# Kernel tuning notes

Measured on AMD Instinct MI355X. Metric: run time of the kernel, lower is better.

The kernel has to match this reference:

```python
import jax, jax.numpy as jnp
import numpy as np

B, S, H, A, V = 128, 128, 1024, 1024, 50000
NEG = -1e11  # mask value used by the original for zero scores (padded positions)


def setup_inputs() -> dict:
    key = jax.random.key(0)
    ks = jax.random.split(key, 10)
    b_ih = jnp.zeros((4 * H,), jnp.float32).at[H:2 * H].set(1.0)  # forget_bias
    b_hh = jnp.zeros((4 * H,), jnp.float32).at[H:2 * H].set(1.0)
    return {
        "input": jax.random.randint(ks[0], (B,), 0, V),
        "prev_h": jax.random.normal(ks[1], (B, H), jnp.float32),
        "prev_c": jax.random.normal(ks[2], (B, H), jnp.float32),
        "encoder_output": jax.random.normal(ks[3], (B, S, H), jnp.float32),
        "emb": jax.random.normal(ks[4], (V, H), jnp.float32) * 0.02,
        "W_ih": jax.random.normal(ks[5], (4 * H, H), jnp.float32) * 0.02,
        "W_hh": jax.random.normal(ks[6], (4 * H, H), jnp.float32) * 0.02,
        "b_ih": b_ih,
        "b_hh": b_hh,
        "W_out": jax.random.normal(ks[7], (A, 2 * H), jnp.float32) * 0.02,
        "b_out": jnp.zeros((A,), jnp.float32),
        "W_out2": jax.random.normal(ks[8], (V, A), jnp.float32) * 0.02,
        "b_out2": jnp.zeros((V,), jnp.float32),
    }


def reference(input, prev_h, prev_c, encoder_output, emb, W_ih, W_hh, b_ih, b_hh,
              W_out, b_out, W_out2, b_out2):
    # embedding lookup (dropout p=0 -> identity)
    x = emb[input]  # [B, H]
    # LSTMCell, PyTorch gate order (i, f, g, o)
    gates = x @ W_ih.T + b_ih + prev_h @ W_hh.T + b_hh  # [B, 4H]
    i, f, g, o = jnp.split(gates, 4, axis=-1)
    c = jax.nn.sigmoid(f) * prev_c + jax.nn.sigmoid(i) * jnp.tanh(g)
    h = jax.nn.sigmoid(o) * jnp.tanh(c)
    # dot attention over (padded) encoder outputs
    scores = jnp.einsum("bsh,bh->bs", encoder_output, h)  # [B, S]
    scores = jnp.where(scores == 0, NEG, scores)          # mask padded rows
    attn = jax.nn.softmax(scores, axis=1)
    context = jnp.einsum("bsh,bs->bh", encoder_output, attn)  # [B, H]
    # MLP decode
    attention_vector = jnp.tanh(jnp.concatenate([context, h], axis=-1) @ W_out.T + b_out)
    logits = attention_vector @ W_out2.T + b_out2  # [B, V]
    output = jax.nn.log_softmax(logits, axis=1)
    return output, h, c
```

## Files before the change

### kernel.cpp

```cpp
#include <hip/hip_runtime.h>
#include <hip/hip_bf16.h>
#include <math.h>

#define Bn 128
#define Sn 128
#define Hn 1024
#define Vn 50000

using short8  = __attribute__((ext_vector_type(8))) short;
using floatx4 = __attribute__((ext_vector_type(4))) float;

__device__ __forceinline__ unsigned short f2bf_bits(float f) {
  union { __hip_bfloat16 h; unsigned short u; } cv;
  cv.h = __float2bfloat16(f);
  return cv.u;
}
__device__ __forceinline__ float bf_bits2f(unsigned short u) {
  union { __hip_bfloat16 h; unsigned short u; } cv;
  cv.u = u;
  return __bfloat162float(cv.h);
}
__device__ __forceinline__ short8 cvt8(float4 a, float4 b) {
  short8 r;
  r[0]=(short)f2bf_bits(a.x); r[1]=(short)f2bf_bits(a.y);
  r[2]=(short)f2bf_bits(a.z); r[3]=(short)f2bf_bits(a.w);
  r[4]=(short)f2bf_bits(b.x); r[5]=(short)f2bf_bits(b.y);
  r[6]=(short)f2bf_bits(b.z); r[7]=(short)f2bf_bits(b.w);
  return r;
}
__device__ __forceinline__ void split8(float4 a, float4 b, short8& hi, short8& lo) {
  float f[8] = {a.x,a.y,a.z,a.w,b.x,b.y,b.z,b.w};
#pragma unroll
  for (int i=0;i<8;++i) {
    unsigned short h = f2bf_bits(f[i]);
    hi[i] = (short)h;
    lo[i] = (short)f2bf_bits(f[i] - bf_bits2f(h));
  }
}
__device__ __forceinline__ floatx4 mfma16(short8 a, short8 b, floatx4 c) {
  return __builtin_amdgcn_mfma_f32_16x16x32_bf16(a, b, c, 0, 0, 0);
}

__global__ void __launch_bounds__(256) k1_pack(const int* __restrict__ inp,
    const float* __restrict__ prev_h, const float* __restrict__ emb,
    unsigned short* __restrict__ xh_hi, unsigned short* __restrict__ xh_lo) {
  int idx = blockIdx.x*256 + threadIdx.x;
  int b = idx >> 11, k = idx & 2047;
  if (k < 1024) {
    float v = emb[(size_t)inp[b]*Hn + k];
    xh_hi[idx] = f2bf_bits(v);
  } else {
    float v = prev_h[b*Hn + (k-1024)];
    unsigned short hi = f2bf_bits(v);
    xh_hi[idx] = hi;
    xh_lo[b*Hn + (k-1024)] = f2bf_bits(v - bf_bits2f(hi));
  }
}

__global__ void __launch_bounds__(64) k2_gates(
    const unsigned short* __restrict__ xh_hi, const unsigned short* __restrict__ xh_lo,
    const float* __restrict__ W_ih, const float* __restrict__ W_hh,
    const float* __restrict__ b_ih, const float* __restrict__ b_hh,
    float* __restrict__ gates) {
  int lane = threadIdx.x, l15 = lane & 15, quad = lane >> 4;
  int n = blockIdx.x*16 + l15;
  floatx4 z = {0.f,0.f,0.f,0.f};
  floatx4 acc[8];
#pragma unroll
  for (int t=0;t<8;++t) acc[t] = z;

  for (int k0 = 0; k0 < 1024; k0 += 32) {
    int k = k0 + quad*8;
    const float* wp = W_ih + (size_t)n*Hn + k;
    float4 w0 = *(const float4*)wp;
    float4 w1 = *(const float4*)(wp+4);
    short8 bfrag = cvt8(w0,w1);
#pragma unroll
    for (int t=0;t<8;++t) {
      short8 afrag = *(const short8*)(xh_hi + (t*16 + l15)*2048 + k);
      acc[t] = mfma16(afrag, bfrag, acc[t]);
    }
  }
  for (int k0 = 0; k0 < 1024; k0 += 32) {
    int k = k0 + quad*8;
    const float* wp = W_hh + (size_t)n*Hn + k;
    float4 w0 = *(const float4*)wp;
    float4 w1 = *(const float4*)(wp+4);
    short8 whi, wlo; split8(w0,w1,whi,wlo);
#pragma unroll
    for (int t=0;t<8;++t) {
      short8 ahi = *(const short8*)(xh_hi + (t*16 + l15)*2048 + 1024 + k);
      short8 alo = *(const short8*)(xh_lo + (t*16 + l15)*1024 + k);
      acc[t] = mfma16(ahi, whi, acc[t]);
      acc[t] = mfma16(alo, whi, acc[t]);
      acc[t] = mfma16(ahi, wlo, acc[t]);
    }
  }
  float bias = b_ih[n] + b_hh[n];
#pragma unroll
  for (int t=0;t<8;++t)
#pragma unroll
    for (int r=0;r<4;++r) {
      int m = t*16 + quad*4 + r;
      gates[m*4096 + n] = acc[t][r] + bias;
    }
}

__global__ void __launch_bounds__(256) k3_lstm(const float* __restrict__ gates,
    const float* __restrict__ prev_c, float* __restrict__ out,
    float* __restrict__ h32, unsigned short* __restrict__ ctxh) {
  int idx = blockIdx.x*256 + threadIdx.x;
  int b = idx >> 10, k = idx & 1023;
  const float* g = gates + b*4096;
  float gi = g[k], gf = g[k+1024], gg = g[k+2048], go = g[k+3072];
  float si = 1.f/(1.f+expf(-gi));
  float sf = 1.f/(1.f+expf(-gf));
  float so = 1.f/(1.f+expf(-go));
  float c = sf*prev_c[idx] + si*tanhf(gg);
  float h = so*tanhf(c);
  out[6400000 + idx] = h;
  out[6531072 + idx] = c;
  h32[idx] = h;
  ctxh[b*2048 + 1024 + k] = f2bf_bits(h);
}

__global__ void __launch_bounds__(256) k4a_scores(const float* __restrict__ enc,
    const float* __restrict__ h32, float* __restrict__ scores) {
  int w = blockIdx.x*4 + (threadIdx.x>>6);
  int lane = threadIdx.x & 63;
  int b = w >> 7, s = w & 127;
  const float* e = enc + (size_t)(b*Sn + s)*Hn;
  const float* hp = h32 + b*Hn;
  float sum = 0.f;
#pragma unroll
  for (int j=0;j<4;++j) {
    int k = j*256 + lane*4;
    float4 ev = *(const float4*)(e+k);
    float4 hv = *(const float4*)(hp+k);
    sum += ev.x*hv.x + ev.y*hv.y + ev.z*hv.z + ev.w*hv.w;
  }
#pragma unroll
  for (int o=32;o>0;o>>=1) sum += __shfl_xor(sum, o, 64);
  if (lane==0) {
    if (sum == 0.f) sum = -1e11f;
    scores[b*Sn+s] = sum;
  }
}

__global__ void __launch_bounds__(256) k4b_ctx(const float* __restrict__ enc,
    const float* __restrict__ scores, unsigned short* __restrict__ ctxh) {
  __shared__ float sc[128];
  __shared__ float red[128];
  int tid = threadIdx.x, b = blockIdx.y;
  if (tid < 128) { float v = scores[b*Sn+tid]; sc[tid] = v; red[tid] = v; }
  __syncthreads();
  for (int st=64; st>0; st>>=1) {
    if (tid<st) red[tid] = fmaxf(red[tid], red[tid+st]);
    __syncthreads();
  }
  float mx = red[0];
  __syncthreads();
  if (tid<128) { float e = expf(sc[tid]-mx); sc[tid]=e; red[tid]=e; }
  __syncthreads();
  for (int st=64; st>0; st>>=1) {
    if (tid<st) red[tid] += red[tid+st];
    __syncthreads();
  }
  float inv = 1.0f/red[0];
  __syncthreads();
  if (tid<128) sc[tid] *= inv;
  __syncthreads();
  int hcol = blockIdx.x*256 + tid;
  const float* e = enc + (size_t)b*(Sn*Hn) + hcol;
  float acc = 0.f;
#pragma unroll 8
  for (int s2=0; s2<128; ++s2) acc += sc[s2]*e[(size_t)s2*Hn];
  ctxh[b*2048 + hcol] = f2bf_bits(acc);
}

__global__ void __launch_bounds__(64) k5_att(const unsigned short* __restrict__ ctxh,
    const float* __restrict__ W_out, const float* __restrict__ b_out,
    unsigned short* __restrict__ av) {
  int lane = threadIdx.x, l15 = lane&15, quad = lane>>6 ? 0 : lane>>4;
  quad = lane >> 4;
  int n = blockIdx.x*16 + l15;
  int mbase = blockIdx.y*64;
  floatx4 z = {0.f,0.f,0.f,0.f};
  floatx4 acc[4];
#pragma unroll
  for (int t=0;t<4;++t) acc[t]=z;
  for (int k0=0;k0<2048;k0+=32) {
    int k = k0 + quad*8;
    const float* wp = W_out + (size_t)n*2048 + k;
    float4 w0=*(const float4*)wp, w1=*(const float4*)(wp+4);
    short8 bfrag = cvt8(w0,w1);
#pragma unroll
    for (int t=0;t<4;++t) {
      short8 afrag = *(const short8*)(ctxh + (mbase + t*16 + l15)*2048 + k);
      acc[t] = mfma16(afrag, bfrag, acc[t]);
    }
  }
  float bias = b_out[n];
#pragma unroll
  for (int t=0;t<4;++t)
#pragma unroll
    for (int r=0;r<4;++r) {
      int m = mbase + t*16 + quad*4 + r;
      av[m*Hn + n] = f2bf_bits(tanhf(acc[t][r] + bias));
    }
}

__global__ void __launch_bounds__(64) k6a_logits(const unsigned short* __restrict__ av,
    const float* __restrict__ W2, const float* __restrict__ b2,
    float* __restrict__ out) {
  int lane = threadIdx.x, l15 = lane&15, quad = lane>>4;
  int v = blockIdx.x*16 + l15;
  floatx4 z = {0.f,0.f,0.f,0.f};
  floatx4 acc[8];
#pragma unroll
  for (int t=0;t<8;++t) acc[t]=z;
  for (int k0=0;k0<1024;k0+=32) {
    int k = k0 + quad*8;
    const float* wp = W2 + (size_t)v*Hn + k;
    float4 w0=*(const float4*)wp, w1=*(const float4*)(wp+4);
    short8 bfrag = cvt8(w0,w1);
#pragma unroll
    for (int t=0;t<8;++t) {
      short8 afrag = *(const short8*)(av + (t*16 + l15)*Hn + k);
      acc[t] = mfma16(afrag, bfrag, acc[t]);
    }
  }
  float bias = b2[v];
#pragma unroll
  for (int t=0;t<8;++t)
#pragma unroll
    for (int r=0;r<4;++r) {
      int m = t*16 + quad*4 + r;
      out[(size_t)m*Vn + v] = acc[t][r] + bias;
    }
}

__global__ void __launch_bounds__(256) k6b_lse(const float* __restrict__ logits,
    float* __restrict__ lse) {
  int b = blockIdx.x, tid = threadIdx.x;
  const float* row = logits + (size_t)b*Vn;
  float m = -3.4e38f, s = 0.f;
  for (int v = tid; v < Vn; v += 256) {
    float x = row[v];
    float nm = fmaxf(m, x);
    s = s*expf(m-nm) + expf(x-nm);
    m = nm;
  }
  __shared__ float sm[256], ss[256];
  sm[tid]=m; ss[tid]=s;
  __syncthreads();
  for (int st=128; st>0; st>>=1) {
    if (tid<st) {
      float m1=sm[tid], m2=sm[tid+st];
      float nm=fmaxf(m1,m2);
      ss[tid]=ss[tid]*expf(m1-nm)+ss[tid+st]*expf(m2-nm);
      sm[tid]=nm;
    }
    __syncthreads();
  }
  if (tid==0) lse[b] = sm[0] + logf(ss[0]);
}

__global__ void __launch_bounds__(256) k6c_sub(float* __restrict__ out,
    const float* __restrict__ lse) {
  int f = blockIdx.x*256 + threadIdx.x;
  if (f >= 12500) return;
  int b = blockIdx.y;
  float l = lse[b];
  float4* p = (float4*)(out + (size_t)b*Vn) + f;
  float4 v = *p;
  v.x -= l; v.y -= l; v.z -= l; v.w -= l;
  *p = v;
}

extern "C" void kernel_launch(void* const* d_in, const int* in_sizes, int n_in,
                              void* d_out, int out_size, void* d_ws, size_t ws_size,
                              hipStream_t stream) {
  const int*   inp    = (const int*)d_in[0];
  const float* prev_h = (const float*)d_in[1];
  const float* prev_c = (const float*)d_in[2];
  const float* enc    = (const float*)d_in[3];
  const float* emb    = (const float*)d_in[4];
  const float* W_ih   = (const float*)d_in[5];
  const float* W_hh   = (const float*)d_in[6];
  const float* b_ih   = (const float*)d_in[7];
  const float* b_hh   = (const float*)d_in[8];
  const float* W_out  = (const float*)d_in[9];
  const float* b_out  = (const float*)d_in[10];
  const float* W_out2 = (const float*)d_in[11];
  const float* b_out2 = (const float*)d_in[12];
  float* out = (float*)d_out;
  char* ws = (char*)d_ws;

  unsigned short* xh_hi = (unsigned short*)(ws + 0);
  unsigned short* xh_lo = (unsigned short*)(ws + 524288);
  float* gates          = (float*)(ws + 786432);
  float* h32            = (float*)(ws + 2883584);
  float* scores         = (float*)(ws + 3407872);
  unsigned short* ctxh  = (unsigned short*)(ws + 3473408);
  unsigned short* av    = (unsigned short*)(ws + 3997696);
  float* lse            = (float*)(ws + 4259840);

  k1_pack   <<<1024, 256, 0, stream>>>(inp, prev_h, emb, xh_hi, xh_lo);
  k2_gates  <<<256, 64, 0, stream>>>(xh_hi, xh_lo, W_ih, W_hh, b_ih, b_hh, gates);
  k3_lstm   <<<512, 256, 0, stream>>>(gates, prev_c, out, h32, ctxh);
  k4a_scores<<<4096, 256, 0, stream>>>(enc, h32, scores);
  k4b_ctx   <<<dim3(4,128), 256, 0, stream>>>(enc, scores, ctxh);
  k5_att    <<<dim3(64,2), 64, 0, stream>>>(ctxh, W_out, b_out, av);
  k6a_logits<<<3125, 64, 0, stream>>>(av, W_out2, b_out2, out);
  k6b_lse   <<<128, 256, 0, stream>>>(out, lse);
  k6c_sub   <<<dim3(49,128), 256, 0, stream>>>(out, lse);
}
```

Baseline: 751.0 us.

## Split GEMM batch tiles across blocks, LDS-tile logits GEMM, two-stage LSE

The gates and attention GEMMs now split the batch dimension across grid blocks, so there are more small blocks in flight, each working on one 16-row tile. The logits GEMM becomes a 256-thread block that stages activation and weight tiles through double-buffered LDS, so one block covers 64 vocabulary columns against all 128 batch rows. The log-sum-exp becomes a two-pass reduction spread over 8 chunks per row, which adds parallelism to a pass that previously ran one block per row. In exchange, the gates and attention kernels reload each weight fragment once per batch tile, which multiplies weight traffic, and the logits loop adds LDS barriers.

```diff
diff --git a/kernel.cpp b/kernel.cpp
--- a/kernel.cpp
+++ b/kernel.cpp
@@ -64,10 +64,8 @@
     float* __restrict__ gates) {
   int lane = threadIdx.x, l15 = lane & 15, quad = lane >> 4;
   int n = blockIdx.x*16 + l15;
-  floatx4 z = {0.f,0.f,0.f,0.f};
-  floatx4 acc[8];
-#pragma unroll
-  for (int t=0;t<8;++t) acc[t] = z;
+  int mt = blockIdx.y;
+  floatx4 acc = {0.f,0.f,0.f,0.f};
 
   for (int k0 = 0; k0 < 1024; k0 += 32) {
     int k = k0 + quad*8;
@@ -75,11 +73,8 @@
     float4 w0 = *(const float4*)wp;
     float4 w1 = *(const float4*)(wp+4);
     short8 bfrag = cvt8(w0,w1);
-#pragma unroll
-    for (int t=0;t<8;++t) {
-      short8 afrag = *(const short8*)(xh_hi + (t*16 + l15)*2048 + k);
-      acc[t] = mfma16(afrag, bfrag, acc[t]);
-    }
+    short8 afrag = *(const short8*)(xh_hi + (mt*16 + l15)*2048 + k);
+    acc = mfma16(afrag, bfrag, acc);
   }
   for (int k0 = 0; k0 < 1024; k0 += 32) {
     int k = k0 + quad*8;
@@ -87,23 +82,18 @@
     float4 w0 = *(const float4*)wp;
     float4 w1 = *(const float4*)(wp+4);
     short8 whi, wlo; split8(w0,w1,whi,wlo);
-#pragma unroll
-    for (int t=0;t<8;++t) {
-      short8 ahi = *(const short8*)(xh_hi + (t*16 + l15)*2048 + 1024 + k);
-      short8 alo = *(const short8*)(xh_lo + (t*16 + l15)*1024 + k);
-      acc[t] = mfma16(ahi, whi, acc[t]);
-      acc[t] = mfma16(alo, whi, acc[t]);
-      acc[t] = mfma16(ahi, wlo, acc[t]);
-    }
+    short8 ahi = *(const short8*)(xh_hi + (mt*16 + l15)*2048 + 1024 + k);
+    short8 alo = *(const short8*)(xh_lo + (mt*16 + l15)*1024 + k);
+    acc = mfma16(ahi, whi, acc);
+    acc = mfma16(alo, whi, acc);
+    acc = mfma16(ahi, wlo, acc);
   }
   float bias = b_ih[n] + b_hh[n];
 #pragma unroll
-  for (int t=0;t<8;++t)
-#pragma unroll
-    for (int r=0;r<4;++r) {
-      int m = t*16 + quad*4 + r;
-      gates[m*4096 + n] = acc[t][r] + bias;
-    }
+  for (int r=0;r<4;++r) {
+    int m = mt*16 + quad*4 + r;
+    gates[m*4096 + n] = acc[r] + bias;
+  }
 }
 
 __global__ void __launch_bounds__(256) k3_lstm(const float* __restrict__ gates,
@@ -181,71 +171,105 @@
 __global__ void __launch_bounds__(64) k5_att(const unsigned short* __restrict__ ctxh,
     const float* __restrict__ W_out, const float* __restrict__ b_out,
     unsigned short* __restrict__ av) {
-  int lane = threadIdx.x, l15 = lane&15, quad = lane>>6 ? 0 : lane>>4;
-  quad = lane >> 4;
+  int lane = threadIdx.x, l15 = lane&15, quad = lane>>4;
   int n = blockIdx.x*16 + l15;
-  int mbase = blockIdx.y*64;
-  floatx4 z = {0.f,0.f,0.f,0.f};
-  floatx4 acc[4];
-#pragma unroll
-  for (int t=0;t<4;++t) acc[t]=z;
+  int mt = blockIdx.y;
+  floatx4 acc = {0.f,0.f,0.f,0.f};
   for (int k0=0;k0<2048;k0+=32) {
     int k = k0 + quad*8;
     const float* wp = W_out + (size_t)n*2048 + k;
     float4 w0=*(const float4*)wp, w1=*(const float4*)(wp+4);
     short8 bfrag = cvt8(w0,w1);
-#pragma unroll
-    for (int t=0;t<4;++t) {
-      short8 afrag = *(const short8*)(ctxh + (mbase + t*16 + l15)*2048 + k);
-      acc[t] = mfma16(afrag, bfrag, acc[t]);
-    }
+    short8 afrag = *(const short8*)(ctxh + (mt*16 + l15)*2048 + k);
+    acc = mfma16(afrag, bfrag, acc);
   }
   float bias = b_out[n];
 #pragma unroll
-  for (int t=0;t<4;++t)
-#pragma unroll
-    for (int r=0;r<4;++r) {
-      int m = mbase + t*16 + quad*4 + r;
-      av[m*Hn + n] = f2bf_bits(tanhf(acc[t][r] + bias));
-    }
-}
-
-__global__ void __launch_bounds__(64) k6a_logits(const unsigned short* __restrict__ av,
+  for (int r=0;r<4;++r) {
+    int m = mt*16 + quad*4 + r;
+    av[m*Hn + n] = f2bf_bits(tanhf(acc[r] + bias));
+  }
+}
+
+__global__ void __launch_bounds__(256) k6a_logits(const unsigned short* __restrict__ av,
     const float* __restrict__ W2, const float* __restrict__ b2,
     float* __restrict__ out) {
-  int lane = threadIdx.x, l15 = lane&15, quad = lane>>4;
-  int v = blockIdx.x*16 + l15;
+  __shared__ unsigned short lA[2][128*40];
+  __shared__ unsigned short lB[2][64*40];
+  int tid = threadIdx.x;
+  int wave = tid>>6, lane = tid&63, l15 = lane&15, quad = lane>>4;
+  int tileN = blockIdx.x*64;
+
+  int arow = tid>>2, apart = tid&3;
+  int brow = tid>>3, bpart = tid&7;
+
+  uint4 aR0, aR1; float4 wR0, wR1;
+
+  auto gload = [&](int k0) {
+    aR0 = *(const uint4*)(av + (size_t)arow*Hn + k0 + apart*8);
+    aR1 = *(const uint4*)(av + (size_t)(arow+64)*Hn + k0 + apart*8);
+    int r0 = tileN + brow;      if (r0 > Vn-1) r0 = Vn-1;
+    int r1 = tileN + brow + 32; if (r1 > Vn-1) r1 = Vn-1;
+    wR0 = *(const float4*)(W2 + (size_t)r0*Hn + k0 + bpart*4);
+    wR1 = *(const float4*)(W2 + (size_t)r1*Hn + k0 + bpart*4);
+  };
+  auto lstore = [&](int buf) {
+    *(uint4*)(&lA[buf][arow*40 + apart*8])      = aR0;
+    *(uint4*)(&lA[buf][(arow+64)*40 + apart*8]) = aR1;
+    ushort4 p0, p1;
+    p0.x=f2bf_bits(wR0.x); p0.y=f2bf_bits(wR0.y); p0.z=f2bf_bits(wR0.z); p0.w=f2bf_bits(wR0.w);
+    p1.x=f2bf_bits(wR1.x); p1.y=f2bf_bits(wR1.y); p1.z=f2bf_bits(wR1.z); p1.w=f2bf_bits(wR1.w);
+    *(ushort4*)(&lB[buf][brow*40 + bpart*4])      = p0;
+    *(ushort4*)(&lB[buf][(brow+32)*40 + bpart*4]) = p1;
+  };
+
   floatx4 z = {0.f,0.f,0.f,0.f};
   floatx4 acc[8];
 #pragma unroll
   for (int t=0;t<8;++t) acc[t]=z;
-  for (int k0=0;k0<1024;k0+=32) {
-    int k = k0 + quad*8;
-    const float* wp = W2 + (size_t)v*Hn + k;
-    float4 w0=*(const float4*)wp, w1=*(const float4*)(wp+4);
-    short8 bfrag = cvt8(w0,w1);
-#pragma unroll
-    for (int t=0;t<8;++t) {
-      short8 afrag = *(const short8*)(av + (t*16 + l15)*Hn + k);
-      acc[t] = mfma16(afrag, bfrag, acc[t]);
+
+  gload(0);
+  lstore(0);
+  __syncthreads();
+
+  for (int kc=0; kc<32; ++kc) {
+    int cur = kc&1;
+    if (kc<31) gload((kc+1)*32);
+    short8 bfrag = *(const short8*)(&lB[cur][(wave*16+l15)*40 + quad*8]);
+    short8 af[8];
+#pragma unroll
+    for (int t=0;t<8;++t)
+      af[t] = *(const short8*)(&lA[cur][(t*16+l15)*40 + quad*8]);
+#pragma unroll
+    for (int t=0;t<8;++t)
+      acc[t] = mfma16(af[t], bfrag, acc[t]);
+    if (kc<31) {
+      __syncthreads();
+      lstore(1-cur);
+      __syncthreads();
     }
   }
-  float bias = b2[v];
-#pragma unroll
-  for (int t=0;t<8;++t)
-#pragma unroll
-    for (int r=0;r<4;++r) {
-      int m = t*16 + quad*4 + r;
-      out[(size_t)m*Vn + v] = acc[t][r] + bias;
-    }
-}
-
-__global__ void __launch_bounds__(256) k6b_lse(const float* __restrict__ logits,
-    float* __restrict__ lse) {
-  int b = blockIdx.x, tid = threadIdx.x;
+
+  int n = tileN + wave*16 + l15;
+  if (n < Vn) {
+    float bias = b2[n];
+#pragma unroll
+    for (int t=0;t<8;++t)
+#pragma unroll
+      for (int r=0;r<4;++r) {
+        int m = t*16 + quad*4 + r;
+        out[(size_t)m*Vn + n] = acc[t][r] + bias;
+      }
+  }
+}
+
+__global__ void __launch_bounds__(256) k6b1_lse(const float* __restrict__ logits,
+    float* __restrict__ pm, float* __restrict__ ps) {
+  int b = blockIdx.y, c = blockIdx.x, tid = threadIdx.x;
+  int v0 = c*6250, v1 = v0 + 6250;
   const float* row = logits + (size_t)b*Vn;
   float m = -3.4e38f, s = 0.f;
-  for (int v = tid; v < Vn; v += 256) {
+  for (int v = v0 + tid; v < v1; v += 256) {
     float x = row[v];
     float nm = fmaxf(m, x);
     s = s*expf(m-nm) + expf(x-nm);
@@ -263,7 +287,21 @@
     }
     __syncthreads();
   }
-  if (tid==0) lse[b] = sm[0] + logf(ss[0]);
+  if (tid==0) { pm[b*8+c]=sm[0]; ps[b*8+c]=ss[0]; }
+}
+
+__global__ void __launch_bounds__(128) k6b2_lse(const float* __restrict__ pm,
+    const float* __restrict__ ps, float* __restrict__ lse) {
+  int b = threadIdx.x;
+  float m = -3.4e38f, s = 0.f;
+#pragma unroll
+  for (int c=0;c<8;++c) {
+    float m2 = pm[b*8+c], s2 = ps[b*8+c];
+    float nm = fmaxf(m, m2);
+    s = s*expf(m-nm) + s2*expf(m2-nm);
+    m = nm;
+  }
+  lse[b] = m + logf(s);
 }
 
 __global__ void __launch_bounds__(256) k6c_sub(float* __restrict__ out,
@@ -305,14 +343,17 @@
   unsigned short* ctxh  = (unsigned short*)(ws + 3473408);
   unsigned short* av    = (unsigned short*)(ws + 3997696);
   float* lse            = (float*)(ws + 4259840);
+  float* pm             = (float*)(ws + 4260352);
+  float* ps             = (float*)(ws + 4264448);
 
   k1_pack   <<<1024, 256, 0, stream>>>(inp, prev_h, emb, xh_hi, xh_lo);
-  k2_gates  <<<256, 64, 0, stream>>>(xh_hi, xh_lo, W_ih, W_hh, b_ih, b_hh, gates);
+  k2_gates  <<<dim3(256,8), 64, 0, stream>>>(xh_hi, xh_lo, W_ih, W_hh, b_ih, b_hh, gates);
   k3_lstm   <<<512, 256, 0, stream>>>(gates, prev_c, out, h32, ctxh);
   k4a_scores<<<4096, 256, 0, stream>>>(enc, h32, scores);
   k4b_ctx   <<<dim3(4,128), 256, 0, stream>>>(enc, scores, ctxh);
-  k5_att    <<<dim3(64,2), 64, 0, stream>>>(ctxh, W_out, b_out, av);
-  k6a_logits<<<3125, 64, 0, stream>>>(av, W_out2, b_out2, out);
-  k6b_lse   <<<128, 256, 0, stream>>>(out, lse);
+  k5_att    <<<dim3(64,8), 64, 0, stream>>>(ctxh, W_out, b_out, av);
+  k6a_logits<<<782, 256, 0, stream>>>(av, W_out2, b_out2, out);
+  k6b1_lse  <<<dim3(8,128), 256, 0, stream>>>(out, pm, ps);
+  k6b2_lse  <<<1, 128, 0, stream>>>(pm, ps, lse);
   k6c_sub   <<<dim3(49,128), 256, 0, stream>>>(out, lse);
 }
```

After: 628.7 us. -16.3%, faster.
